# Performance work log

Measured on AMD Instinct MI355X. Metric: run time of the kernel, lower is better.

Reference implementation:

```python
import jax, jax.numpy as jnp
import numpy as np

NUM_SEGMENTS = 4480  # BATCH_SIZE * MAX_ATOMS = 64 * 70
ATOM_DIM = 64
BOND_DIM = 16
N_EDGES = 65536


def setup_inputs() -> dict:
    key = jax.random.key(0)
    k1, k2, k3, k4 = jax.random.split(key, 4)
    atom_feat = jax.random.normal(k1, (NUM_SEGMENTS, ATOM_DIM), dtype=jnp.float32)
    bond_feat = jax.random.normal(k2, (N_EDGES, BOND_DIM), dtype=jnp.float32)
    pair_idx = jax.random.randint(k3, (N_EDGES, 2), 0, NUM_SEGMENTS, dtype=jnp.int64)
    # glorot-uniform style kernel, zero bias (as in add_weight initializers)
    limit = float(np.sqrt(6.0 / (BOND_DIM + ATOM_DIM ** 2)))
    kernel = jax.random.uniform(k4, (BOND_DIM, ATOM_DIM ** 2), dtype=jnp.float32,
                                minval=-limit, maxval=limit)
    bias = jnp.zeros((ATOM_DIM ** 2,), dtype=jnp.float32)
    return {"atom_feat": atom_feat, "bond_feat": bond_feat,
            "pair_idx": pair_idx, "kernel": kernel, "bias": bias}


def reference(atom_feat, bond_feat, pair_idx, kernel, bias):
    atom_dim = atom_feat.shape[-1]
    # dense projection of bond features -> per-edge transform matrices
    bond_transformed = bond_feat @ kernel + bias               # [E, D*D]
    bond_transformed = bond_transformed.reshape(-1, atom_dim, atom_dim)  # [E, D, D]
    # gather neighbor (source) atom features per edge
    neighbor_feat = jnp.take(atom_feat, pair_idx[:, 1].astype(jnp.int32), axis=0)  # [E, D]
    # per-edge matrix-vector product
    messages = jnp.einsum('eij,ej->ei', bond_transformed, neighbor_feat)  # [E, D]
    # scatter-add into destination atoms
    return jax.ops.segment_sum(messages, pair_idx[:, 0].astype(jnp.int32),
                               num_segments=NUM_SEGMENTS)  # [NUM_SEGMENTS, D]
```

## Files before the change

kernel.cpp:

```cpp
#include <hip/hip_runtime.h>

#define NSEG   4480
#define ADIM   64
#define BDIM   16
#define NEDGE  65536
#define DPB    16
#define NBLK   (NSEG / DPB)
#define TPB    512
#define CAP    64
#define GSP    1096
#define ALP    68

#define CNT_OFF  (4u << 20)

typedef __bf16 bf16x8 __attribute__((ext_vector_type(8)));
typedef float  f32x4  __attribute__((ext_vector_type(4)));

__device__ __forceinline__ unsigned short f2bf(float f) {
    union { float f; unsigned int i; } c; c.f = f;
    unsigned int x = c.i;
    x += 0x7fffu + ((x >> 16) & 1u);
    return (unsigned short)(x >> 16);
}

union U8 { unsigned short u[8]; bf16x8 v; };

__device__ __forceinline__ bf16x8 pack_bf8(float4 a, float4 b) {
    U8 r;
    r.u[0] = f2bf(a.x); r.u[1] = f2bf(a.y); r.u[2] = f2bf(a.z); r.u[3] = f2bf(a.w);
    r.u[4] = f2bf(b.x); r.u[5] = f2bf(b.y); r.u[6] = f2bf(b.z); r.u[7] = f2bf(b.w);
    return r.v;
}

__device__ __forceinline__ float rl(float v, int l) {
    return __builtin_bit_cast(float,
        __builtin_amdgcn_readlane(__builtin_bit_cast(int, v), l));
}

__global__ __launch_bounds__(256) void scatter_kernel(
    const int* __restrict__ pair, int* __restrict__ cnt, int2* __restrict__ eb)
{
    const int e  = blockIdx.x * 256 + threadIdx.x;
    const int2 p = ((const int2*)pair)[e];
    const int idx = atomicAdd(&cnt[p.x], 1);
    if (idx < CAP) eb[(size_t)p.x * CAP + idx] = make_int2(e, p.y);
}

__global__ __launch_bounds__(TPB, 4) void fused_kernel(
    const float* __restrict__ atom,
    const float* __restrict__ bond,
    const int*   __restrict__ cnt,
    const int2*  __restrict__ eb,
    const float* __restrict__ kern,
    const float* __restrict__ bias,
    float*       __restrict__ out)
{
    __shared__ unsigned short Gs[DPB * GSP];
    __shared__ float Al[8][16 * ALP];
    __shared__ f32x4 pb[4][64];

    const int t    = threadIdx.x;
    const int lane = t & 63;
    const int w    = t >> 6;
    const int dlo  = blockIdx.x * DPB;
    const int q    = lane >> 2;
    const int p    = lane & 3;
    float* myAl = Al[w];

#pragma unroll
    for (int half = 0; half < 2; ++half) {
        const int dl = 2 * w + half;
        const int d  = dlo + dl;
        int n = cnt[d]; n = n < CAP ? n : CAP;

        float g[17];
#pragma unroll
        for (int r = 0; r < 17; ++r) g[r] = 0.f;

        for (int kb = 0; kb < n; kb += 16) {
            const int  slot = kb + q;
            const bool val  = slot < n;
            const int2 es   = eb[(size_t)d * CAP + (val ? slot : 0)];
            const float vs  = val ? 1.f : 0.f;

            const float* ap = atom + (size_t)es.y * ADIM + p * 16;
            float4 a0 = ((const float4*)ap)[0];
            float4 a1 = ((const float4*)ap)[1];
            float4 a2 = ((const float4*)ap)[2];
            float4 a3 = ((const float4*)ap)[3];
            const float4 bq = ((const float4*)(bond + (size_t)es.x * BDIM))[p];

            a0.x *= vs; a0.y *= vs; a0.z *= vs; a0.w *= vs;
            a1.x *= vs; a1.y *= vs; a1.z *= vs; a1.w *= vs;
            a2.x *= vs; a2.y *= vs; a2.z *= vs; a2.w *= vs;
            a3.x *= vs; a3.y *= vs; a3.z *= vs; a3.w *= vs;

            float* dst = myAl + q * ALP + p * 16;
            ((float4*)dst)[0] = a0;
            ((float4*)dst)[1] = a1;
            ((float4*)dst)[2] = a2;
            ((float4*)dst)[3] = a3;
            __asm__ __volatile__("s_waitcnt lgkmcnt(0)" ::: "memory");

#pragma unroll
            for (int qq = 0; qq < 16; ++qq) {
                const float a = myAl[qq * ALP + lane];
                g[16] += a;
#pragma unroll
                for (int pp = 0; pp < 4; ++pp) {
                    const int sl = 4 * qq + pp;
                    g[pp * 4 + 0] = fmaf(rl(bq.x, sl), a, g[pp * 4 + 0]);
                    g[pp * 4 + 1] = fmaf(rl(bq.y, sl), a, g[pp * 4 + 1]);
                    g[pp * 4 + 2] = fmaf(rl(bq.z, sl), a, g[pp * 4 + 2]);
                    g[pp * 4 + 3] = fmaf(rl(bq.w, sl), a, g[pp * 4 + 3]);
                }
            }
        }

#pragma unroll
        for (int r = 0; r < 17; ++r)
            Gs[dl * GSP + r * 64 + lane] = f2bf(g[r]);
    }
    __syncthreads();

    {
        const int kh   = w >> 2;
        const int ct   = w & 3;
        const int m    = lane & 15;
        const int quad = lane >> 4;
        const int c    = ct * 16 + m;
        const unsigned short* Ga = Gs + (size_t)m * GSP;
        const int rlo = kh ? 9 : 0;
        const int rhi = kh ? 17 : 9;

        f32x4 acc = {0.f, 0.f, 0.f, 0.f};

        const float* ks0 = ((rlo < 16) ? (kern + (size_t)rlo * 4096) : bias)
                           + (size_t)c * 64 + quad * 8;
        float4 x0 = *(const float4*)(ks0);
        float4 x1 = *(const float4*)(ks0 + 4);
        float4 y0 = *(const float4*)(ks0 + 32);
        float4 y1 = *(const float4*)(ks0 + 36);

        for (int r = rlo; r < rhi; ++r) {
            float4 nx0 = {}, nx1 = {}, ny0 = {}, ny1 = {};
            if (r + 1 < rhi) {
                const float* ns = ((r + 1 < 16) ? (kern + (size_t)(r + 1) * 4096)
                                                : bias)
                                  + (size_t)c * 64 + quad * 8;
                nx0 = *(const float4*)(ns);
                nx1 = *(const float4*)(ns + 4);
                ny0 = *(const float4*)(ns + 32);
                ny1 = *(const float4*)(ns + 36);
            }
            const bf16x8 a0 = *(const bf16x8*)(Ga + r * 64 + quad * 8);
            const bf16x8 a1 = *(const bf16x8*)(Ga + r * 64 + 32 + quad * 8);
            acc = __builtin_amdgcn_mfma_f32_16x16x32_bf16(a0, pack_bf8(x0, x1), acc, 0, 0, 0);
            acc = __builtin_amdgcn_mfma_f32_16x16x32_bf16(a1, pack_bf8(y0, y1), acc, 0, 0, 0);
            x0 = nx0; x1 = nx1; y0 = ny0; y1 = ny1;
        }

        if (kh) pb[ct][lane] = acc;
        __syncthreads();
        if (!kh) {
            const f32x4 pr = pb[ct][lane];
            acc[0] += pr[0]; acc[1] += pr[1]; acc[2] += pr[2]; acc[3] += pr[3];
#pragma unroll
            for (int rr = 0; rr < 4; ++rr)
                out[(size_t)(dlo + quad * 4 + rr) * ADIM + c] = acc[rr];
        }
    }
}

extern "C" void kernel_launch(void* const* d_in, const int* in_sizes, int n_in,
                              void* d_out, int out_size, void* d_ws, size_t ws_size,
                              hipStream_t stream) {
    const float* atom = (const float*)d_in[0];
    const float* bond = (const float*)d_in[1];
    const int*   pair = (const int*)  d_in[2];
    const float* kern = (const float*)d_in[3];
    const float* bias = (const float*)d_in[4];
    float* out = (float*)d_out;

    int2* eb  = (int2*)d_ws;
    int*  cnt = (int*)((char*)d_ws + CNT_OFF);

    hipMemsetAsync(cnt, 0, NSEG * sizeof(int), stream);
    scatter_kernel<<<NEDGE / 256, 256, 0, stream>>>(pair, cnt, eb);
    fused_kernel<<<NBLK, TPB, 0, stream>>>(atom, bond, cnt, eb, kern, bias, out);
}
```

Measured before the change: 97.73 us.

## Fuse edge binning into main kernel with per-block LDS scan and cache warmup

New measurement: 109.8 us. 1.12x slower.

```diff
diff --git a/kernel.cpp b/kernel.cpp
--- a/kernel.cpp
+++ b/kernel.cpp
@@ -8,10 +8,9 @@
 #define NBLK   (NSEG / DPB)
 #define TPB    512
 #define CAP    64
-#define GSP    1096
-#define ALP    68
-
-#define CNT_OFF  (4u << 20)
+#define GSP    1092
+#define ALP    66
+
 
 typedef __bf16 bf16x8 __attribute__((ext_vector_type(8)));
 typedef float  f32x4  __attribute__((ext_vector_type(4)));
@@ -37,32 +36,63 @@
         __builtin_amdgcn_readlane(__builtin_bit_cast(int, v), l));
 }
 
-__global__ __launch_bounds__(256) void scatter_kernel(
-    const int* __restrict__ pair, int* __restrict__ cnt, int2* __restrict__ eb)
-{
-    const int e  = blockIdx.x * 256 + threadIdx.x;
-    const int2 p = ((const int2*)pair)[e];
-    const int idx = atomicAdd(&cnt[p.x], 1);
-    if (idx < CAP) eb[(size_t)p.x * CAP + idx] = make_int2(e, p.y);
-}
-
 __global__ __launch_bounds__(TPB, 4) void fused_kernel(
     const float* __restrict__ atom,
     const float* __restrict__ bond,
-    const int*   __restrict__ cnt,
-    const int2*  __restrict__ eb,
+    const int*   __restrict__ pair,
     const float* __restrict__ kern,
     const float* __restrict__ bias,
     float*       __restrict__ out)
 {
+    __shared__ int  bcnt[DPB];
+    __shared__ int2 ebuf[DPB][CAP];
     __shared__ unsigned short Gs[DPB * GSP];
     __shared__ float Al[8][16 * ALP];
     __shared__ f32x4 pb[4][64];
 
-    const int t    = threadIdx.x;
+    const int t   = threadIdx.x;
+    const int dlo = blockIdx.x * DPB;
+
+    if (t < DPB) bcnt[t] = 0;
+
+    {
+        float s = 0.f;
+        const int g0 = blockIdx.x * TPB + t;
+        const int gs = NBLK * TPB;
+        const float4* a4 = (const float4*)atom;
+        const float4* b4 = (const float4*)bond;
+        const float4* k4 = (const float4*)kern;
+        const float4* s4 = (const float4*)bias;
+        for (int i = g0; i < 71680;  i += gs) { float4 v = a4[i]; s += v.x + v.y + v.z + v.w; }
+        for (int i = g0; i < 262144; i += gs) { float4 v = b4[i]; s += v.x + v.y + v.z + v.w; }
+        for (int i = g0; i < 16384;  i += gs) { float4 v = k4[i]; s += v.x + v.y + v.z + v.w; }
+        if (g0 < 1024)                          { float4 v = s4[g0]; s += v.x + v.y + v.z + v.w; }
+        __asm__ __volatile__("" :: "v"(s));
+    }
+    __syncthreads();
+
+    {
+        const int4* p4 = (const int4*)pair;
+#pragma unroll 8
+        for (int i = 0; i < NEDGE / 2 / TPB; ++i) {
+            const int  ix4 = i * TPB + t;
+            const int4 pp  = p4[ix4];
+            const unsigned d0 = (unsigned)(pp.x - dlo);
+            if (d0 < DPB) {
+                const int ix = atomicAdd(&bcnt[d0], 1);
+                if (ix < CAP) ebuf[d0][ix] = make_int2(2 * ix4, pp.y);
+            }
+            const unsigned d1 = (unsigned)(pp.z - dlo);
+            if (d1 < DPB) {
+                const int ix = atomicAdd(&bcnt[d1], 1);
+                if (ix < CAP) ebuf[d1][ix] = make_int2(2 * ix4 + 1, pp.w);
+            }
+        }
+    }
+    __syncthreads();
+
     const int lane = t & 63;
     const int w    = t >> 6;
-    const int dlo  = blockIdx.x * DPB;
     const int q    = lane >> 2;
     const int p    = lane & 3;
     float* myAl = Al[w];
@@ -70,8 +100,7 @@
 #pragma unroll
     for (int half = 0; half < 2; ++half) {
         const int dl = 2 * w + half;
-        const int d  = dlo + dl;
-        int n = cnt[d]; n = n < CAP ? n : CAP;
+        int n = bcnt[dl]; n = n < CAP ? n : CAP;
 
         float g[17];
 #pragma unroll
@@ -80,7 +109,7 @@
         for (int kb = 0; kb < n; kb += 16) {
             const int  slot = kb + q;
             const bool val  = slot < n;
-            const int2 es   = eb[(size_t)d * CAP + (val ? slot : 0)];
+            const int2 es   = ebuf[dl][val ? slot : 0];
             const float vs  = val ? 1.f : 0.f;
 
             const float* ap = atom + (size_t)es.y * ADIM + p * 16;
@@ -182,10 +211,5 @@
     const float* bias = (const float*)d_in[4];
     float* out = (float*)d_out;
 
-    int2* eb  = (int2*)d_ws;
-    int*  cnt = (int*)((char*)d_ws + CNT_OFF);
-
-    hipMemsetAsync(cnt, 0, NSEG * sizeof(int), stream);
-    scatter_kernel<<<NEDGE / 256, 256, 0, stream>>>(pair, cnt, eb);
-    fused_kernel<<<NBLK, TPB, 0, stream>>>(atom, bond, cnt, eb, kern, bias, out);
-}
+    fused_kernel<<<NBLK, TPB, 0, stream>>>(atom, bond, pair, kern, bias, out);
+}
```

## Use one wave per destination atom with readlane edge indices and 4-way K split

Applied to the files above, without the earlier changes.

New measurement: 104.0 us. 6.4% more time.

```diff
diff --git a/kernel.cpp b/kernel.cpp
--- a/kernel.cpp
+++ b/kernel.cpp
@@ -6,10 +6,9 @@
 #define NEDGE  65536
 #define DPB    16
 #define NBLK   (NSEG / DPB)
-#define TPB    512
+#define TPB    1024
 #define CAP    64
-#define GSP    1096
-#define ALP    68
+#define GSP    1092
 
 #define CNT_OFF  (4u << 20)
 
@@ -32,11 +31,6 @@
     return r.v;
 }
 
-__device__ __forceinline__ float rl(float v, int l) {
-    return __builtin_bit_cast(float,
-        __builtin_amdgcn_readlane(__builtin_bit_cast(int, v), l));
-}
-
 __global__ __launch_bounds__(256) void scatter_kernel(
     const int* __restrict__ pair, int* __restrict__ cnt, int2* __restrict__ eb)
 {
@@ -46,7 +40,16 @@
     if (idx < CAP) eb[(size_t)p.x * CAP + idx] = make_int2(e, p.y);
 }
 
-__global__ __launch_bounds__(TPB, 4) void fused_kernel(
+__device__ __forceinline__ void edge_fma(float* g, const float4* bp, float a) {
+    const float4 c0 = bp[0], c1 = bp[1], c2 = bp[2], c3 = bp[3];
+    const float bb[16] = { c0.x,c0.y,c0.z,c0.w, c1.x,c1.y,c1.z,c1.w,
+                           c2.x,c2.y,c2.z,c2.w, c3.x,c3.y,c3.z,c3.w };
+#pragma unroll
+    for (int r = 0; r < 16; ++r) g[r] = fmaf(bb[r], a, g[r]);
+    g[16] += a;
+}
+
+__global__ __launch_bounds__(TPB, 1) void fused_kernel(
     const float* __restrict__ atom,
     const float* __restrict__ bond,
     const int*   __restrict__ cnt,
@@ -56,70 +59,63 @@
     float*       __restrict__ out)
 {
     __shared__ unsigned short Gs[DPB * GSP];
-    __shared__ float Al[8][16 * ALP];
-    __shared__ f32x4 pb[4][64];
+    __shared__ f32x4 pb[3][4][64];
 
     const int t    = threadIdx.x;
     const int lane = t & 63;
     const int w    = t >> 6;
     const int dlo  = blockIdx.x * DPB;
-    const int q    = lane >> 2;
-    const int p    = lane & 3;
-    float* myAl = Al[w];
+    const int d    = dlo + w;
 
-#pragma unroll
-    for (int half = 0; half < 2; ++half) {
-        const int dl = 2 * w + half;
-        const int d  = dlo + dl;
+    {
         int n = cnt[d]; n = n < CAP ? n : CAP;
+        const int2 my = eb[(size_t)d * CAP + lane];
 
         float g[17];
 #pragma unroll
         for (int r = 0; r < 17; ++r) g[r] = 0.f;
 
         for (int kb = 0; kb < n; kb += 16) {
-            const int  slot = kb + q;
-            const bool val  = slot < n;
-            const int2 es   = eb[(size_t)d * CAP + (val ? slot : 0)];
-            const float vs  = val ? 1.f : 0.f;
+#pragma unroll
+            for (int c4 = 0; c4 < 4; ++c4) {
+                const int s0 = kb + c4 * 4;
+                if (s0 >= n) break;
+                const bool v0 = true;
+                const bool v1 = s0 + 1 < n;
+                const bool v2 = s0 + 2 < n;
+                const bool v3 = s0 + 3 < n;
+                int e0 = __builtin_amdgcn_readlane(my.x, s0);
+                int y0 = __builtin_amdgcn_readlane(my.y, s0);
+                int e1 = __builtin_amdgcn_readlane(my.x, s0 + 1);
+                int y1 = __builtin_amdgcn_readlane(my.y, s0 + 1);
+                int e2 = __builtin_amdgcn_readlane(my.x, s0 + 2);
+                int y2 = __builtin_amdgcn_readlane(my.y, s0 + 2);
+                int e3 = __builtin_amdgcn_readlane(my.x, s0 + 3);
+                int y3 = __builtin_amdgcn_readlane(my.y, s0 + 3);
+                e1 = v1 ? e1 : 0;  y1 = v1 ? y1 : 0;
+                e2 = v2 ? e2 : 0;  y2 = v2 ? y2 : 0;
+                e3 = v3 ? e3 : 0;  y3 = v3 ? y3 : 0;
 
-            const float* ap = atom + (size_t)es.y * ADIM + p * 16;
-            float4 a0 = ((const float4*)ap)[0];
-            float4 a1 = ((const float4*)ap)[1];
-            float4 a2 = ((const float4*)ap)[2];
-            float4 a3 = ((const float4*)ap)[3];
-            const float4 bq = ((const float4*)(bond + (size_t)es.x * BDIM))[p];
+                const float a0 = atom[(size_t)y0 * ADIM + lane];
+                const float a1 = atom[(size_t)y1 * ADIM + lane] * (v1 ? 1.f : 0.f);
+                const float a2 = atom[(size_t)y2 * ADIM + lane] * (v2 ? 1.f : 0.f);
+                const float a3 = atom[(size_t)y3 * ADIM + lane] * (v3 ? 1.f : 0.f);
+                const float4* b0 = (const float4*)(bond + (size_t)e0 * BDIM);
+                const float4* b1 = (const float4*)(bond + (size_t)e1 * BDIM);
+                const float4* b2 = (const float4*)(bond + (size_t)e2 * BDIM);
+                const float4* b3 = (const float4*)(bond + (size_t)e3 * BDIM);
 
-            a0.x *= vs; a0.y *= vs; a0.z *= vs; a0.w *= vs;
-            a1.x *= vs; a1.y *= vs; a1.z *= vs; a1.w *= vs;
-            a2.x *= vs; a2.y *= vs; a2.z *= vs; a2.w *= vs;
-            a3.x *= vs; a3.y *= vs; a3.z *= vs; a3.w *= vs;
-
-            float* dst = myAl + q * ALP + p * 16;
-            ((float4*)dst)[0] = a0;
-            ((float4*)dst)[1] = a1;
-            ((float4*)dst)[2] = a2;
-            ((float4*)dst)[3] = a3;
-            __asm__ __volatile__("s_waitcnt lgkmcnt(0)" ::: "memory");
-
-#pragma unroll
-            for (int qq = 0; qq < 16; ++qq) {
-                const float a = myAl[qq * ALP + lane];
-                g[16] += a;
-#pragma unroll
-                for (int pp = 0; pp < 4; ++pp) {
-                    const int sl = 4 * qq + pp;
-                    g[pp * 4 + 0] = fmaf(rl(bq.x, sl), a, g[pp * 4 + 0]);
-                    g[pp * 4 + 1] = fmaf(rl(bq.y, sl), a, g[pp * 4 + 1]);
-                    g[pp * 4 + 2] = fmaf(rl(bq.z, sl), a, g[pp * 4 + 2]);
-                    g[pp * 4 + 3] = fmaf(rl(bq.w, sl), a, g[pp * 4 + 3]);
-                }
+                edge_fma(g, b0, a0);
+                edge_fma(g, b1, a1);
+                edge_fma(g, b2, a2);
+                edge_fma(g, b3, a3);
+                (void)v0;
             }
         }
 
 #pragma unroll
         for (int r = 0; r < 17; ++r)
-            Gs[dl * GSP + r * 64 + lane] = f2bf(g[r]);
+            Gs[w * GSP + r * 64 + lane] = f2bf(g[r]);
     }
     __syncthreads();
 
@@ -130,8 +126,8 @@
         const int quad = lane >> 4;
         const int c    = ct * 16 + m;
         const unsigned short* Ga = Gs + (size_t)m * GSP;
-        const int rlo = kh ? 9 : 0;
-        const int rhi = kh ? 17 : 9;
+        const int rlo = (kh == 0) ? 0 : (kh == 1) ? 5 : (kh == 2) ? 9  : 13;
+        const int rhi = (kh == 0) ? 5 : (kh == 1) ? 9 : (kh == 2) ? 13 : 17;
 
         f32x4 acc = {0.f, 0.f, 0.f, 0.f};
 
@@ -160,11 +156,14 @@
             x0 = nx0; x1 = nx1; y0 = ny0; y1 = ny1;
         }
 
-        if (kh) pb[ct][lane] = acc;
+        if (kh) pb[kh - 1][ct][lane] = acc;
         __syncthreads();
-        if (!kh) {
-            const f32x4 pr = pb[ct][lane];
-            acc[0] += pr[0]; acc[1] += pr[1]; acc[2] += pr[2]; acc[3] += pr[3];
+        if (kh == 0) {
+#pragma unroll
+            for (int i = 0; i < 3; ++i) {
+                const f32x4 pr = pb[i][ct][lane];
+                acc[0] += pr[0]; acc[1] += pr[1]; acc[2] += pr[2]; acc[3] += pr[3];
+            }
 #pragma unroll
             for (int rr = 0; rr < 4; ++rr)
                 out[(size_t)(dlo + quad * 4 + rr) * ADIM + c] = acc[rr];
```
